# Performance work log

Hardware: AMD Instinct MI355X
Metric: run time of the kernel (lower is better)

## Reference

```python
import jax, jax.numpy as jnp
import numpy as np

EPS = 1e-7
MAX_TANH = 1.0 - 1e-6  # clamp for arctanh stability


def _norm(v):
    # last-axis L2 norm, clamped away from zero
    return jnp.maximum(jnp.linalg.norm(v, axis=-1, keepdims=True), EPS)


def log_map_zero(y):
    # Poincare ball (c=1) log map at the origin
    n = _norm(y)
    return jnp.arctanh(jnp.clip(n, 0.0, MAX_TANH)) * y / n


def exp_map_zero(v):
    # Poincare ball (c=1) exp map at the origin
    n = _norm(v)
    return jnp.tanh(n) * v / n


def h_add(x, y):
    # Mobius addition x (+) y on the Poincare ball (c=1)
    xy = jnp.sum(x * y, axis=-1, keepdims=True)
    x2 = jnp.sum(x * x, axis=-1, keepdims=True)
    y2 = jnp.sum(y * y, axis=-1, keepdims=True)
    num = (1.0 + 2.0 * xy + y2) * x + (1.0 - x2) * y
    den = 1.0 + 2.0 * xy + x2 * y2
    return num / jnp.maximum(den, EPS)


def h_mul(x, W):
    # Mobius matrix-vector multiply: exp0( log0(x) @ W )
    return exp_map_zero(log_map_zero(x) @ W)


def setup_inputs() -> dict:
    key = jax.random.key(0)
    k1, k2, k3, k4 = jax.random.split(key, 4)
    N, F_IN, F_OUT = 8192, 128, 128
    # node features inside the unit ball: ||x|| ~ 0.05*sqrt(128) ~ 0.57
    x = 0.05 * jax.random.normal(k1, (N, F_IN), dtype=jnp.float32)
    # sparse-ish row-normalized dense adjacency
    a = (jax.random.uniform(k2, (N, N)) < 0.01).astype(jnp.float32)
    adj = a / jnp.maximum(a.sum(axis=1, keepdims=True), 1.0)
    # xavier-uniform-ish weights
    lim_e = np.sqrt(6.0 / (F_IN + F_IN)) * np.sqrt(2.0)
    lim_l = np.sqrt(6.0 / (2 * F_IN + F_OUT)) * np.sqrt(2.0)
    embed = jax.random.uniform(k3, (F_IN, F_IN), minval=-lim_e, maxval=lim_e, dtype=jnp.float32)
    layer = jax.random.uniform(k4, (2 * F_IN, F_OUT), minval=-lim_l, maxval=lim_l, dtype=jnp.float32)
    embed_bias = jnp.zeros((F_IN,), dtype=jnp.float32)
    layer_bias = jnp.zeros((F_OUT,), dtype=jnp.float32)
    return {"x": x, "adj": adj, "embed": embed, "layer": layer,
            "embed_bias": embed_bias, "layer_bias": layer_bias}


def reference(x, adj, embed, layer, embed_bias, layer_bias):
    # h = (embed (x)mobius x) (+) embed_bias
    h = h_mul(x, embed)                      # [N, F_IN]
    h = h_add(h, embed_bias[None, :])
    # neighbor aggregation in tangent space at origin
    neigh = exp_map_zero(adj @ log_map_zero(h))   # [N, F_IN]
    # out = (layer (x)mobius [x ; neigh]) (+) layer_bias
    out = h_mul(jnp.concatenate((x, neigh), axis=1), layer)  # [N, F_OUT]
    out = h_add(out, layer_bias[None, :])
    return out
```

## Files before the change

### kernel.cpp

```cpp
#include <hip/hip_runtime.h>
#include <math.h>

#define EPS  1e-7f
#define MAXT 0.999999f

typedef short  s16x8  __attribute__((ext_vector_type(8)));
typedef float  f32x16 __attribute__((ext_vector_type(16)));

__device__ __forceinline__ float waveRedSum(float v) {
    #pragma unroll
    for (int off = 32; off > 0; off >>= 1)
        v += __shfl_xor(v, off, 64);
    return v;
}

__device__ __forceinline__ unsigned short f2bf(float f) {
    unsigned u = __float_as_uint(f);
    u += 0x7fff + ((u >> 16) & 1);
    return (unsigned short)(u >> 16);
}

__global__ __launch_bounds__(256) void kA(const float* __restrict__ x,
                                          const float* __restrict__ embed,
                                          const float* __restrict__ ebias,
                                          unsigned short* __restrict__ vpack) {
    __shared__ float u[4][128];
    const int wave = threadIdx.x >> 6;
    const int lane = threadIdx.x & 63;
    const int row  = blockIdx.x * 4 + wave;
    const int c0   = lane * 2;

    const float2 xr = *(const float2*)(x + (size_t)row * 128 + c0);

    float n2 = waveRedSum(xr.x * xr.x + xr.y * xr.y);
    float n  = fmaxf(sqrtf(n2), EPS);
    float sc = atanhf(fminf(n, MAXT)) / n;
    u[wave][c0]     = xr.x * sc;
    u[wave][c0 + 1] = xr.y * sc;
    __syncthreads();

    float a0 = 0.f, a1 = 0.f;
    #pragma unroll 8
    for (int k = 0; k < 128; k++) {
        float  uk = u[wave][k];
        float2 e  = *(const float2*)(embed + (size_t)k * 128 + c0);
        a0 = fmaf(uk, e.x, a0);
        a1 = fmaf(uk, e.y, a1);
    }

    float np2 = waveRedSum(a0 * a0 + a1 * a1);
    float np  = fmaxf(sqrtf(np2), EPS);
    float se  = tanhf(np) / np;
    float h0 = a0 * se, h1 = a1 * se;
    float x2 = np2 * se * se;

    float bx = ebias[c0], by = ebias[c0 + 1];
    float xy = waveRedSum(h0 * bx + h1 * by);
    float y2 = waveRedSum(bx * bx + by * by);
    float den = fmaxf(1.f + 2.f * xy + x2 * y2, EPS);
    float cx = 1.f + 2.f * xy + y2;
    float cy = 1.f - x2;
    float hb0 = (cx * h0 + cy * bx) / den;
    float hb1 = (cx * h1 + cy * by) / den;

    float m2 = waveRedSum(hb0 * hb0 + hb1 * hb1);
    float m  = fmaxf(sqrtf(m2), EPS);
    float sl = atanhf(fminf(m, MAXT)) / m;
    float v0 = hb0 * sl, v1 = hb1 * sl;

    const int tbase = (row >> 4) * 2048 + (row & 15);
    vpack[tbase + c0 * 16]       = f2bf(v0);
    vpack[tbase + (c0 + 1) * 16] = f2bf(v1);
}

#define BK 128

__global__ __launch_bounds__(256) void kB(const float* __restrict__ adj,
                                          const unsigned short* __restrict__ vpack,
                                          float* __restrict__ tpart,
                                          int klen) {
    __shared__ __align__(16) unsigned short As[32][BK + 8];

    const int tid  = threadIdx.x;
    const int wave = tid >> 6;
    const int lane = tid & 63;
    const int r0   = blockIdx.x * 32;
    const int k0   = blockIdx.y * klen;
    float* tout    = tpart + (size_t)blockIdx.y * 8192 * 128;

    const int srow = tid >> 3;
    const int scol = (tid & 7) * 16;
    const float* aptr = adj + (size_t)(r0 + srow) * 8192 + k0 + scol;

    const int m  = lane & 31;
    const int kh = lane >> 5;
    const int n  = wave * 32 + m;
    const unsigned short* vb = vpack + (size_t)n * 16 + kh * 8;

    f32x16 acc = {0.f};

    float4 f0 = *(const float4*)(aptr + 0);
    float4 f1 = *(const float4*)(aptr + 4);
    float4 f2 = *(const float4*)(aptr + 8);
    float4 f3 = *(const float4*)(aptr + 12);

    const int kiters = klen / BK;
    for (int it = 0; it < kiters; it++) {
        __syncthreads();

        union { unsigned short u[8]; s16x8 v; } p0, p1;
        p0.u[0] = f2bf(f0.x); p0.u[1] = f2bf(f0.y); p0.u[2] = f2bf(f0.z); p0.u[3] = f2bf(f0.w);
        p0.u[4] = f2bf(f1.x); p0.u[5] = f2bf(f1.y); p0.u[6] = f2bf(f1.z); p0.u[7] = f2bf(f1.w);
        p1.u[0] = f2bf(f2.x); p1.u[1] = f2bf(f2.y); p1.u[2] = f2bf(f2.z); p1.u[3] = f2bf(f2.w);
        p1.u[4] = f2bf(f3.x); p1.u[5] = f2bf(f3.y); p1.u[6] = f2bf(f3.z); p1.u[7] = f2bf(f3.w);
        *(s16x8*)&As[srow][scol]     = p0.v;
        *(s16x8*)&As[srow][scol + 8] = p1.v;
        __syncthreads();

        if (it + 1 < kiters) {
            aptr += BK;
            f0 = *(const float4*)(aptr + 0);
            f1 = *(const float4*)(aptr + 4);
            f2 = *(const float4*)(aptr + 8);
            f3 = *(const float4*)(aptr + 12);
        }

        const int ktile0 = (k0 + it * BK) >> 4;
        #pragma unroll
        for (int kk = 0; kk < BK / 16; kk++) {
            s16x8 a = *(const s16x8*)&As[m][kk * 16 + kh * 8];
            s16x8 b = *(const s16x8*)(vb + (size_t)(ktile0 + kk) * 2048);
            acc = __builtin_amdgcn_mfma_f32_32x32x16_bf16(a, b, acc, 0, 0, 0);
        }
    }

    #pragma unroll
    for (int r = 0; r < 16; r++) {
        int row = r0 + (r & 3) + 8 * (r >> 2) + 4 * kh;
        tout[(size_t)row * 128 + n] = acc[r];
    }
}

__global__ __launch_bounds__(256) void kC(const float* __restrict__ x,
                                          const float* __restrict__ tpart,
                                          const float* __restrict__ layer,
                                          const float* __restrict__ lbias,
                                          float* __restrict__ out,
                                          int S) {
    __shared__ float w[4][256];
    const int wave = threadIdx.x >> 6;
    const int lane = threadIdx.x & 63;
    const int row  = blockIdx.x * 4 + wave;
    const int c0   = lane * 2;

    float2 tr = *(const float2*)(tpart + (size_t)row * 128 + c0);
    for (int s = 1; s < S; s++) {
        float2 p = *(const float2*)(tpart + (size_t)s * 8192 * 128 + (size_t)row * 128 + c0);
        tr.x += p.x; tr.y += p.y;
    }
    const float2 xr = *(const float2*)(x + (size_t)row * 128 + c0);

    float st = waveRedSum(tr.x * tr.x + tr.y * tr.y);
    float sx = waveRedSum(xr.x * xr.x + xr.y * xr.y);

    float nt = fmaxf(sqrtf(st), EPS);
    float se = tanhf(nt) / nt;

    float ncat2 = sx + st * se * se;
    float ncat  = fmaxf(sqrtf(ncat2), EPS);
    float sw    = atanhf(fminf(ncat, MAXT)) / ncat;
    w[wave][c0]           = xr.x * sw;
    w[wave][c0 + 1]       = xr.y * sw;
    w[wave][128 + c0]     = tr.x * se * sw;
    w[wave][128 + c0 + 1] = tr.y * se * sw;
    __syncthreads();

    float a0 = 0.f, a1 = 0.f;
    #pragma unroll 8
    for (int k = 0; k < 256; k++) {
        float  wk = w[wave][k];
        float2 e  = *(const float2*)(layer + (size_t)k * 128 + c0);
        a0 = fmaf(wk, e.x, a0);
        a1 = fmaf(wk, e.y, a1);
    }

    float np2 = waveRedSum(a0 * a0 + a1 * a1);
    float np  = fmaxf(sqrtf(np2), EPS);
    float so  = tanhf(np) / np;
    float o0 = a0 * so, o1 = a1 * so;
    float x2 = np2 * so * so;

    float bx = lbias[c0], by = lbias[c0 + 1];
    float xy = waveRedSum(o0 * bx + o1 * by);
    float y2 = waveRedSum(bx * bx + by * by);
    float den = fmaxf(1.f + 2.f * xy + x2 * y2, EPS);
    float cx = 1.f + 2.f * xy + y2;
    float cy = 1.f - x2;

    float2 res;
    res.x = (cx * o0 + cy * bx) / den;
    res.y = (cx * o1 + cy * by) / den;
    *(float2*)(out + (size_t)row * 128 + c0) = res;
}

extern "C" void kernel_launch(void* const* d_in, const int* in_sizes, int n_in,
                              void* d_out, int out_size, void* d_ws, size_t ws_size,
                              hipStream_t stream) {
    const float* x     = (const float*)d_in[0];
    const float* adj   = (const float*)d_in[1];
    const float* embed = (const float*)d_in[2];
    const float* layer = (const float*)d_in[3];
    const float* eb    = (const float*)d_in[4];
    const float* lb    = (const float*)d_in[5];
    float* out = (float*)d_out;

    const size_t vbytes = (size_t)8192 * 128 * 2;
    const size_t slice  = (size_t)8192 * 128 * 4;

    int S = 1;
    if      (ws_size >= vbytes + 8 * slice) S = 8;
    else if (ws_size >= vbytes + 4 * slice) S = 4;
    else if (ws_size >= vbytes + 2 * slice) S = 2;

    unsigned short* vpack = (unsigned short*)d_ws;
    float* tpart = (float*)((char*)d_ws + vbytes);

    kA<<<2048, 256, 0, stream>>>(x, embed, eb, vpack);
    kB<<<dim3(256, S), 256, 0, stream>>>(adj, vpack, tpart, 8192 / S);
    kC<<<2048, 256, 0, stream>>>(x, tpart, layer, lb, out, S);
}
```

Measured before the change: 499.3 us.

## Restructure adjacency GEMM so each wave owns a 32x128 tile without LDS staging

The aggregation kernel now gives each wave its own 32-row by 128-column output tile, with four MFMA accumulators. Each wave loads its adjacency fragment straight from global memory into registers, converting to bf16 in place, so the shared-memory staging and the two barriers per step are gone. Each adjacency element is now read by one wave rather than reused across four waves through LDS, and loads are prefetched one 16-wide k-step ahead. The grid shrinks to 64 blocks per split, and the split-K factor can rise to 16 when the workspace allows, which adds more partial-sum traffic for the final kernel to reduce.

```diff
diff --git a/kernel.cpp b/kernel.cpp
--- a/kernel.cpp
+++ b/kernel.cpp
@@ -73,71 +73,66 @@
     vpack[tbase + (c0 + 1) * 16] = f2bf(v1);
 }
 
-#define BK 128
+__device__ __forceinline__ void kb_chunk(const float4& ca0, const float4& ca1,
+                                         const unsigned short* bp,
+                                         f32x16& acc0, f32x16& acc1,
+                                         f32x16& acc2, f32x16& acc3) {
+    s16x8 b0 = *(const s16x8*)(bp);
+    s16x8 b1 = *(const s16x8*)(bp + 32 * 16);
+    s16x8 b2 = *(const s16x8*)(bp + 64 * 16);
+    s16x8 b3 = *(const s16x8*)(bp + 96 * 16);
+    union { unsigned short u[8]; s16x8 v; } af;
+    af.u[0] = f2bf(ca0.x); af.u[1] = f2bf(ca0.y);
+    af.u[2] = f2bf(ca0.z); af.u[3] = f2bf(ca0.w);
+    af.u[4] = f2bf(ca1.x); af.u[5] = f2bf(ca1.y);
+    af.u[6] = f2bf(ca1.z); af.u[7] = f2bf(ca1.w);
+    acc0 = __builtin_amdgcn_mfma_f32_32x32x16_bf16(af.v, b0, acc0, 0, 0, 0);
+    acc1 = __builtin_amdgcn_mfma_f32_32x32x16_bf16(af.v, b1, acc1, 0, 0, 0);
+    acc2 = __builtin_amdgcn_mfma_f32_32x32x16_bf16(af.v, b2, acc2, 0, 0, 0);
+    acc3 = __builtin_amdgcn_mfma_f32_32x32x16_bf16(af.v, b3, acc3, 0, 0, 0);
+}
 
 __global__ __launch_bounds__(256) void kB(const float* __restrict__ adj,
                                           const unsigned short* __restrict__ vpack,
                                           float* __restrict__ tpart,
                                           int klen) {
-    __shared__ __align__(16) unsigned short As[32][BK + 8];
-
-    const int tid  = threadIdx.x;
-    const int wave = tid >> 6;
-    const int lane = tid & 63;
-    const int r0   = blockIdx.x * 32;
+    const int wave = threadIdx.x >> 6;
+    const int lane = threadIdx.x & 63;
+    const int rt   = blockIdx.x * 4 + wave;
+    const int r0   = rt * 32;
     const int k0   = blockIdx.y * klen;
-    float* tout    = tpart + (size_t)blockIdx.y * 8192 * 128;
-
-    const int srow = tid >> 3;
-    const int scol = (tid & 7) * 16;
-    const float* aptr = adj + (size_t)(r0 + srow) * 8192 + k0 + scol;
+    float* tout    = tpart + (size_t)blockIdx.y * (8192 * 128);
 
     const int m  = lane & 31;
     const int kh = lane >> 5;
-    const int n  = wave * 32 + m;
-    const unsigned short* vb = vpack + (size_t)n * 16 + kh * 8;
-
-    f32x16 acc = {0.f};
-
-    float4 f0 = *(const float4*)(aptr + 0);
-    float4 f1 = *(const float4*)(aptr + 4);
-    float4 f2 = *(const float4*)(aptr + 8);
-    float4 f3 = *(const float4*)(aptr + 12);
-
-    const int kiters = klen / BK;
-    for (int it = 0; it < kiters; it++) {
-        __syncthreads();
-
-        union { unsigned short u[8]; s16x8 v; } p0, p1;
-        p0.u[0] = f2bf(f0.x); p0.u[1] = f2bf(f0.y); p0.u[2] = f2bf(f0.z); p0.u[3] = f2bf(f0.w);
-        p0.u[4] = f2bf(f1.x); p0.u[5] = f2bf(f1.y); p0.u[6] = f2bf(f1.z); p0.u[7] = f2bf(f1.w);
-        p1.u[0] = f2bf(f2.x); p1.u[1] = f2bf(f2.y); p1.u[2] = f2bf(f2.z); p1.u[3] = f2bf(f2.w);
-        p1.u[4] = f2bf(f3.x); p1.u[5] = f2bf(f3.y); p1.u[6] = f2bf(f3.z); p1.u[7] = f2bf(f3.w);
-        *(s16x8*)&As[srow][scol]     = p0.v;
-        *(s16x8*)&As[srow][scol + 8] = p1.v;
-        __syncthreads();
-
-        if (it + 1 < kiters) {
-            aptr += BK;
-            f0 = *(const float4*)(aptr + 0);
-            f1 = *(const float4*)(aptr + 4);
-            f2 = *(const float4*)(aptr + 8);
-            f3 = *(const float4*)(aptr + 12);
-        }
-
-        const int ktile0 = (k0 + it * BK) >> 4;
-        #pragma unroll
-        for (int kk = 0; kk < BK / 16; kk++) {
-            s16x8 a = *(const s16x8*)&As[m][kk * 16 + kh * 8];
-            s16x8 b = *(const s16x8*)(vb + (size_t)(ktile0 + kk) * 2048);
-            acc = __builtin_amdgcn_mfma_f32_32x32x16_bf16(a, b, acc, 0, 0, 0);
-        }
-    }
+
+    const float* aptr = adj + (size_t)(r0 + m) * 8192 + k0 + kh * 8;
+    const unsigned short* bbase = vpack + (size_t)(k0 >> 4) * 2048 + m * 16 + kh * 8;
+
+    f32x16 acc0 = {0.f}, acc1 = {0.f}, acc2 = {0.f}, acc3 = {0.f};
+
+    const int kiters = klen >> 4;
+
+    float4 a0 = *(const float4*)(aptr);
+    float4 a1 = *(const float4*)(aptr + 4);
+
+    for (int kt = 0; kt < kiters - 1; ++kt) {
+        float4 ca0 = a0, ca1 = a1;
+        aptr += 16;
+        a0 = *(const float4*)(aptr);
+        a1 = *(const float4*)(aptr + 4);
+        kb_chunk(ca0, ca1, bbase + (size_t)kt * 2048, acc0, acc1, acc2, acc3);
+    }
+    kb_chunk(a0, a1, bbase + (size_t)(kiters - 1) * 2048, acc0, acc1, acc2, acc3);
 
     #pragma unroll
-    for (int r = 0; r < 16; r++) {
-        int row = r0 + (r & 3) + 8 * (r >> 2) + 4 * kh;
-        tout[(size_t)row * 128 + n] = acc[r];
+    for (int r = 0; r < 16; ++r) {
+        int row  = r0 + (r & 3) + 8 * (r >> 2) + 4 * kh;
+        float* o = tout + (size_t)row * 128 + m;
+        o[0]  = acc0[r];
+        o[32] = acc1[r];
+        o[64] = acc2[r];
+        o[96] = acc3[r];
     }
 }
 
@@ -218,14 +213,15 @@
     const size_t slice  = (size_t)8192 * 128 * 4;
 
     int S = 1;
-    if      (ws_size >= vbytes + 8 * slice) S = 8;
-    else if (ws_size >= vbytes + 4 * slice) S = 4;
-    else if (ws_size >= vbytes + 2 * slice) S = 2;
+    if      (ws_size >= vbytes + 16 * slice) S = 16;
+    else if (ws_size >= vbytes +  8 * slice) S = 8;
+    else if (ws_size >= vbytes +  4 * slice) S = 4;
+    else if (ws_size >= vbytes +  2 * slice) S = 2;
 
     unsigned short* vpack = (unsigned short*)d_ws;
     float* tpart = (float*)((char*)d_ws + vbytes);
 
     kA<<<2048, 256, 0, stream>>>(x, embed, eb, vpack);
-    kB<<<dim3(256, S), 256, 0, stream>>>(adj, vpack, tpart, 8192 / S);
+    kB<<<dim3(64, S), 256, 0, stream>>>(adj, vpack, tpart, 8192 / S);
     kC<<<2048, 256, 0, stream>>>(x, tpart, layer, lb, out, S);
 }
```

Measured after the change: 519.5 us. 1.04x slower.
